# Kernel tuning notes

Hardware: AMD Instinct MI355X
Metric: run time of the kernel (lower is better)

Reference implementation:

```python
import jax, jax.numpy as jnp
import numpy as np

B, S, D_IN, D_OUT = 4, 2048, 2048, 8192


def setup_inputs() -> dict:
    key = jax.random.key(0)
    k1, k2 = jax.random.split(key)
    x = jax.random.normal(k1, (B, S, D_IN), dtype=jnp.float32)
    weight = jax.random.normal(k2, (D_OUT, D_IN), dtype=jnp.float32) * 0.02
    alpha = jnp.float32(1.0)
    bias = jnp.zeros((D_OUT,), dtype=jnp.float32)
    return {"x": x, "weight": weight, "alpha": alpha, "bias": bias}


def reference(x, weight, alpha, bias):
    # Ternary quantization: delta = 0.7 * mean(|w|); w_q in {-1,0,1} * alpha
    delta = 0.7 * jnp.mean(jnp.abs(weight))
    w_t = jnp.where(weight > delta, jnp.float32(1.0),
                    jnp.where(weight < -delta, jnp.float32(-1.0), jnp.float32(0.0)))
    w_q = w_t * alpha  # [out, in]
    # F.linear: x @ w_q^T + bias
    return jnp.einsum('bsd,od->bso', x, w_q) + bias
```

## Files before the change

kernel.cpp:

```cpp
#include <hip/hip_runtime.h>
#include <hip/hip_bf16.h>
#include <stdint.h>

typedef __attribute__((ext_vector_type(4))) int i32x4;
typedef __attribute__((ext_vector_type(16))) int i32x16;
typedef signed char s8;

#define M_TOT 8192
#define N_TOT 8192
#define K_TOT 2048
#define W_COUNT (N_TOT * K_TOT)
#define X_COUNT (M_TOT * K_TOT)

__global__ void tl_reduce(const float* __restrict__ w, const float* __restrict__ x,
                          double* __restrict__ wsum, float* __restrict__ xmax) {
    const int b = blockIdx.x;
    if (b < 1024) {
        const int tid = b * 256 + threadIdx.x;
        const float4* w4 = (const float4*)w;
        double s = 0.0;
        for (int i = tid; i < W_COUNT / 4; i += 1024 * 256) {
            float4 v = w4[i];
            s += (double)fabsf(v.x) + (double)fabsf(v.y) + (double)fabsf(v.z) + (double)fabsf(v.w);
        }
        #pragma unroll
        for (int off = 32; off > 0; off >>= 1) s += __shfl_down(s, off);
        __shared__ double red[4];
        if ((threadIdx.x & 63) == 0) red[threadIdx.x >> 6] = s;
        __syncthreads();
        if (threadIdx.x == 0) wsum[b] = (red[0] + red[1]) + (red[2] + red[3]);
    } else {
        const int tid = (b - 1024) * 256 + threadIdx.x;
        const float4* x4 = (const float4*)x;
        float m = 0.0f;
        for (int i = tid; i < X_COUNT / 4; i += 1024 * 256) {
            float4 v = x4[i];
            m = fmaxf(m, fmaxf(fmaxf(fabsf(v.x), fabsf(v.y)), fmaxf(fabsf(v.z), fabsf(v.w))));
        }
        #pragma unroll
        for (int off = 32; off > 0; off >>= 1) m = fmaxf(m, __shfl_down(m, off));
        __shared__ float redm[4];
        if ((threadIdx.x & 63) == 0) redm[threadIdx.x >> 6] = m;
        __syncthreads();
        if (threadIdx.x == 0) xmax[b - 1024] = fmaxf(fmaxf(redm[0], redm[1]), fmaxf(redm[2], redm[3]));
    }
}

__global__ void tl_finalize(const double* __restrict__ wsum, const float* __restrict__ xmax,
                            const float* __restrict__ alpha,
                            double* __restrict__ delta, float* __restrict__ qp) {
    const int t = threadIdx.x;
    double s = (wsum[t] + wsum[t + 256]) + (wsum[t + 512] + wsum[t + 768]);
    float m = fmaxf(fmaxf(xmax[t], xmax[t + 256]), fmaxf(xmax[t + 512], xmax[t + 768]));
    #pragma unroll
    for (int off = 32; off > 0; off >>= 1) {
        s += __shfl_down(s, off);
        m = fmaxf(m, __shfl_down(m, off));
    }
    __shared__ double rs[4];
    __shared__ float rm[4];
    if ((t & 63) == 0) { rs[t >> 6] = s; rm[t >> 6] = m; }
    __syncthreads();
    if (t == 0) {
        *delta = 0.7 * (((rs[0] + rs[1]) + (rs[2] + rs[3])) / (double)W_COUNT);
        float mm = fmaxf(fmaxf(rm[0], rm[1]), fmaxf(rm[2], rm[3]));
        qp[0] = 127.0f / mm;
        qp[1] = alpha[0] * (mm / 127.0f);
    }
}

__global__ void tl_tern_w(const float* __restrict__ w, const double* __restrict__ delta_p,
                          s8* __restrict__ wb) {
    const double d = *delta_p;
    const int i = (blockIdx.x * 256 + threadIdx.x) * 16;
    union { s8 c[16]; i32x4 v; } o;
    #pragma unroll
    for (int j = 0; j < 16; j += 4) {
        float4 v = *(const float4*)(w + i + j);
        float f[4] = {v.x, v.y, v.z, v.w};
        #pragma unroll
        for (int r = 0; r < 4; ++r) {
            double wd = (double)f[r];
            o.c[j + r] = wd > d ? 1 : (wd < -d ? -1 : 0);
        }
    }
    *(i32x4*)(wb + i) = o.v;
}

__global__ void tl_quant_x(const float* __restrict__ x, const float* __restrict__ qp,
                           s8* __restrict__ xb) {
    const float inv = qp[0];
    const int i = (blockIdx.x * 256 + threadIdx.x) * 16;
    union { s8 c[16]; i32x4 v; } o;
    #pragma unroll
    for (int j = 0; j < 16; j += 4) {
        float4 v = *(const float4*)(x + i + j);
        float f[4] = {v.x, v.y, v.z, v.w};
        #pragma unroll
        for (int r = 0; r < 4; ++r) {
            int q = (int)__builtin_rintf(f[r] * inv);
            q = q > 127 ? 127 : (q < -127 ? -127 : q);
            o.c[j + r] = (s8)q;
        }
    }
    *(i32x4*)(xb + i) = o.v;
}


#define SB    __builtin_amdgcn_sched_barrier(0)
#define BARR  __builtin_amdgcn_s_barrier()
#define LGKM0 asm volatile("s_waitcnt lgkmcnt(0)" ::: "memory")
#define VMW(N) asm volatile("s_waitcnt vmcnt(" #N ")" ::: "memory")

#define GLDS(SRC, DOFF) __builtin_amdgcn_global_load_lds(                      \
    (const __attribute__((address_space(1))) void*)(SRC),                      \
    (__attribute__((address_space(3))) void*)(lds + (DOFF)), 16, 0, 0)

#define RD_A(S, KK) do {                                                       \
    _Pragma("unroll") for (int m_ = 0; m_ < 4; ++m_)                           \
        aF[m_] = *(const i32x4*)(lds + (S) * 16384 + wrOff + m_ * 2048 +       \
                                 (lrd ^ ((KK) * 32)));                         \
} while (0)

#define RD_B(S, KK) do {                                                       \
    _Pragma("unroll") for (int n_ = 0; n_ < 2; ++n_)                           \
        bF[n_] = *(const i32x4*)(lds + 49152 + (S) * 16384 + wcOff + n_ * 2048 + \
                                 (lrd ^ ((KK) * 32)));                         \
} while (0)

#define MM() do {                                                              \
    _Pragma("unroll") for (int m_ = 0; m_ < 4; ++m_)                           \
    _Pragma("unroll") for (int n_ = 0; n_ < 2; ++n_)                           \
        acc[m_][n_] = __builtin_amdgcn_mfma_i32_32x32x32_i8(                   \
            aF[m_], bF[n_], acc[m_][n_], 0, 0, 0);                             \
} while (0)

#define KTILE(S, SSTG, KOFF, DOSTG, GATE) do {                                 \
                            \
    RD_A(S, 0); RD_B(S, 0);                                                    \
    if (DOSTG) { GLDS(aSrc + (KOFF), (SSTG) * 16384 + L);                      \
                 GLDS(aSrc + (KOFF) + 262144, (SSTG) * 16384 + 8192 + L); }    \
    SB; BARR; LGKM0; SB;                                                       \
    __builtin_amdgcn_s_setprio(1); MM(); __builtin_amdgcn_s_setprio(0); SB; BARR; \
                                        \
    RD_A(S, 1); RD_B(S, 1);                                                    \
    if (DOSTG) { GLDS(bSrc + (KOFF), 49152 + (SSTG) * 16384 + L);              \
                 GLDS(bSrc + (KOFF) + 262144, 49152 + (SSTG) * 16384 + 8192 + L); } \
    SB; BARR; LGKM0; SB;                                                       \
    __builtin_amdgcn_s_setprio(1); MM(); __builtin_amdgcn_s_setprio(0); SB;    \
    GATE; BARR;                                                                \
} while (0)

__global__ __launch_bounds__(512, 1) void tl_gemm_i8(
    const s8* __restrict__ A, const s8* __restrict__ Bm,
    const float* __restrict__ qp, const float* __restrict__ bias,
    float* __restrict__ C) {
    __shared__ __attribute__((aligned(128))) char lds[98304];

    const int t = threadIdx.x;
    const int wid = t >> 6;
    const int l = t & 63;
    const int wr = wid >> 2;
    const int wc = wid & 3;

    const int bid = blockIdx.x;
    const int x = bid & 7;
    const int j = bid >> 3;
    const int tm = x * 4 + ((j >> 3) & 3);
    const int tn = (j >> 5) * 8 + (j & 7);
    const int row0 = tm * 256, col0 = tn * 256;

    const int L = t * 16;
    const int off = L ^ (((L >> 7) & 3) << 4);
    const int sr = off >> 6;
    const int kb = off & 63;
    const s8* aSrc = A + (size_t)(row0 + sr) * K_TOT + kb;
    const s8* bSrc = Bm + (size_t)(col0 + sr) * K_TOT + kb;

    const int rl = l & 31, kg = l >> 5;
    const int lrd = rl * 64 + ((kg ^ ((rl >> 1) & 3)) << 4);
    const int wrOff = wr * 8192;
    const int wcOff = wc * 4096;

    i32x16 acc[4][2] = {};
    i32x4 aF[4], bF[2];

    GLDS(aSrc, L);                    GLDS(aSrc + 262144, 8192 + L);
    GLDS(bSrc, 49152 + L);            GLDS(bSrc + 262144, 49152 + 8192 + L);
    GLDS(aSrc + 64, 16384 + L);       GLDS(aSrc + 64 + 262144, 16384 + 8192 + L);
    GLDS(bSrc + 64, 49152 + 16384 + L);
    GLDS(bSrc + 64 + 262144, 49152 + 16384 + 8192 + L);
    VMW(4); BARR;

    int koff = 128;
    #pragma unroll 1
    for (int i = 0; i < 10; ++i) {
        KTILE(0, 2, koff, 1, VMW(4)); koff += 64;
        KTILE(1, 0, koff, 1, VMW(4)); koff += 64;
        KTILE(2, 1, koff, 1, VMW(4)); koff += 64;
    }
    KTILE(0, 0, 0, 0, VMW(0));
    KTILE(1, 0, 0, 0, (void)0);

    const float osc = qp[1];
    #pragma unroll
    for (int m_ = 0; m_ < 4; ++m_) {
        const int crow = row0 + wr * 128 + m_ * 32 + kg * 4;
        #pragma unroll
        for (int n_ = 0; n_ < 2; ++n_) {
            const int ccol = col0 + wc * 64 + n_ * 32 + rl;
            const float bv = bias[ccol];
            #pragma unroll
            for (int r = 0; r < 16; ++r) {
                const int row = crow + (r & 3) + 8 * (r >> 2);
                C[(size_t)row * N_TOT + ccol] = (float)acc[m_][n_][r] * osc + bv;
            }
        }
    }
}

extern "C" void kernel_launch(void* const* d_in, const int* in_sizes, int n_in,
                              void* d_out, int out_size, void* d_ws, size_t ws_size,
                              hipStream_t stream) {
    const float* x     = (const float*)d_in[0];
    const float* wgt   = (const float*)d_in[1];
    const float* alpha = (const float*)d_in[2];
    const float* bias  = (const float*)d_in[3];
    float* out = (float*)d_out;

    char* ws = (char*)d_ws;
    double* wsum = (double*)ws;
    float* xmax  = (float*)(ws + 8192);
    double* delta = (double*)(ws + 12288);
    float* qp     = (float*)(ws + 12304);
    s8* xb = (s8*)(ws + 16384);
    s8* wb = (s8*)(ws + 16384 + (size_t)X_COUNT);

    tl_reduce<<<2048, 256, 0, stream>>>(wgt, x, wsum, xmax);
    tl_finalize<<<1, 256, 0, stream>>>(wsum, xmax, alpha, delta, qp);
    tl_tern_w<<<W_COUNT / (256 * 16), 256, 0, stream>>>(wgt, delta, wb);
    tl_quant_x<<<X_COUNT / (256 * 16), 256, 0, stream>>>(x, qp, xb);
    tl_gemm_i8<<<(M_TOT / 256) * (N_TOT / 256), 512, 0, stream>>>(xb, wb, qp, bias, out);
}
```

Before: 212.3 us.

## Double-buffer LDS fragments in registers and cut barriers per K tile

Restructures the int8 GEMM main loop so the LDS fragment reads for the next half-tile are issued while the MFMAs for the current one run. Fragments are held in two register sets (aP/bP and aN/bN), and a partial lgkmcnt(6) wait replaces full drains. Each K tile now has a single barrier instead of four, with A and B staging issued together after it. In exchange the loop waits for all outstanding global loads each tile, which shortens the prefetch distance. Launch bounds are also raised to 2 blocks per CU, which caps registers next to the 128-register accumulator and risks spills, even though the 96KB LDS per block likely prevents two blocks from fitting.

```diff
diff --git a/kernel.cpp b/kernel.cpp
--- a/kernel.cpp
+++ b/kernel.cpp
@@ -109,49 +109,52 @@
 
 #define SB    __builtin_amdgcn_sched_barrier(0)
 #define BARR  __builtin_amdgcn_s_barrier()
+#define LGKM6 asm volatile("s_waitcnt lgkmcnt(6)" ::: "memory")
 #define LGKM0 asm volatile("s_waitcnt lgkmcnt(0)" ::: "memory")
 #define VMW(N) asm volatile("s_waitcnt vmcnt(" #N ")" ::: "memory")
+#define PRIO1 __builtin_amdgcn_s_setprio(1)
+#define PRIO0 __builtin_amdgcn_s_setprio(0)
 
 #define GLDS(SRC, DOFF) __builtin_amdgcn_global_load_lds(                      \
     (const __attribute__((address_space(1))) void*)(SRC),                      \
     (__attribute__((address_space(3))) void*)(lds + (DOFF)), 16, 0, 0)
 
-#define RD_A(S, KK) do {                                                       \
+#define READ6(AR, BR, S, KK) do {                                              \
     _Pragma("unroll") for (int m_ = 0; m_ < 4; ++m_)                           \
-        aF[m_] = *(const i32x4*)(lds + (S) * 16384 + wrOff + m_ * 2048 +       \
+        AR[m_] = *(const i32x4*)(lds + (S) * 16384 + wrOff + m_ * 2048 +       \
                                  (lrd ^ ((KK) * 32)));                         \
-} while (0)
-
-#define RD_B(S, KK) do {                                                       \
     _Pragma("unroll") for (int n_ = 0; n_ < 2; ++n_)                           \
-        bF[n_] = *(const i32x4*)(lds + 49152 + (S) * 16384 + wcOff + n_ * 2048 + \
+        BR[n_] = *(const i32x4*)(lds + 49152 + (S) * 16384 + wcOff + n_ * 2048 + \
                                  (lrd ^ ((KK) * 32)));                         \
 } while (0)
 
-#define MM() do {                                                              \
+#define MMX(AR, BR) do {                                                       \
     _Pragma("unroll") for (int m_ = 0; m_ < 4; ++m_)                           \
     _Pragma("unroll") for (int n_ = 0; n_ < 2; ++n_)                           \
         acc[m_][n_] = __builtin_amdgcn_mfma_i32_32x32x32_i8(                   \
-            aF[m_], bF[n_], acc[m_][n_], 0, 0, 0);                             \
-} while (0)
-
-#define KTILE(S, SSTG, KOFF, DOSTG, GATE) do {                                 \
-                            \
-    RD_A(S, 0); RD_B(S, 0);                                                    \
-    if (DOSTG) { GLDS(aSrc + (KOFF), (SSTG) * 16384 + L);                      \
-                 GLDS(aSrc + (KOFF) + 262144, (SSTG) * 16384 + 8192 + L); }    \
-    SB; BARR; LGKM0; SB;                                                       \
-    __builtin_amdgcn_s_setprio(1); MM(); __builtin_amdgcn_s_setprio(0); SB; BARR; \
-                                        \
-    RD_A(S, 1); RD_B(S, 1);                                                    \
-    if (DOSTG) { GLDS(bSrc + (KOFF), 49152 + (SSTG) * 16384 + L);              \
-                 GLDS(bSrc + (KOFF) + 262144, 49152 + (SSTG) * 16384 + 8192 + L); } \
-    SB; BARR; LGKM0; SB;                                                       \
-    __builtin_amdgcn_s_setprio(1); MM(); __builtin_amdgcn_s_setprio(0); SB;    \
-    GATE; BARR;                                                                \
-} while (0)
-
-__global__ __launch_bounds__(512, 1) void tl_gemm_i8(
+            AR[m_], BR[n_], acc[m_][n_], 0, 0, 0);                             \
+} while (0)
+
+#define STG_A(SS, KOFF) do {                                                   \
+    GLDS(aSrc + (KOFF), (SS) * 16384 + L);                                     \
+    GLDS(aSrc + (KOFF) + 262144, (SS) * 16384 + 8192 + L);                     \
+} while (0)
+#define STG_B(SS, KOFF) do {                                                   \
+    GLDS(bSrc + (KOFF), 49152 + (SS) * 16384 + L);                             \
+    GLDS(bSrc + (KOFF) + 262144, 49152 + (SS) * 16384 + 8192 + L);             \
+} while (0)
+
+#define TILE(S, SN, SG, KOFF, DOSTG, LAST) do {                                \
+    READ6(aN, bN, S, 1);                                                       \
+    LGKM6; SB; PRIO1; MMX(aP, bP); PRIO0; SB;                                  \
+    VMW(0); BARR; SB;                                                          \
+    if (!(LAST)) READ6(aP, bP, SN, 0);                                         \
+    if (DOSTG) { STG_A(SG, KOFF); STG_B(SG, KOFF); }                           \
+    if (LAST) { LGKM0; } else { LGKM6; }                                       \
+    SB; PRIO1; MMX(aN, bN); PRIO0; SB;                                         \
+} while (0)
+
+__global__ __launch_bounds__(512, 2) void tl_gemm_i8(
     const s8* __restrict__ A, const s8* __restrict__ Bm,
     const float* __restrict__ qp, const float* __restrict__ bias,
     float* __restrict__ C) {
@@ -164,9 +167,9 @@
     const int wc = wid & 3;
 
     const int bid = blockIdx.x;
-    const int x = bid & 7;
+    const int xc = bid & 7;
     const int j = bid >> 3;
-    const int tm = x * 4 + ((j >> 3) & 3);
+    const int tm = xc * 4 + ((j >> 3) & 3);
     const int tn = (j >> 5) * 8 + (j & 7);
     const int row0 = tm * 256, col0 = tn * 256;
 
@@ -183,24 +186,22 @@
     const int wcOff = wc * 4096;
 
     i32x16 acc[4][2] = {};
-    i32x4 aF[4], bF[2];
-
-    GLDS(aSrc, L);                    GLDS(aSrc + 262144, 8192 + L);
-    GLDS(bSrc, 49152 + L);            GLDS(bSrc + 262144, 49152 + 8192 + L);
-    GLDS(aSrc + 64, 16384 + L);       GLDS(aSrc + 64 + 262144, 16384 + 8192 + L);
-    GLDS(bSrc + 64, 49152 + 16384 + L);
-    GLDS(bSrc + 64 + 262144, 49152 + 16384 + 8192 + L);
-    VMW(4); BARR;
+    i32x4 aP[4], bP[2], aN[4], bN[2];
+
+    STG_A(0, 0); STG_B(0, 0);
+    STG_A(1, 64); STG_B(1, 64);
+    VMW(4); BARR; SB;
+    READ6(aP, bP, 0, 0);
 
     int koff = 128;
     #pragma unroll 1
     for (int i = 0; i < 10; ++i) {
-        KTILE(0, 2, koff, 1, VMW(4)); koff += 64;
-        KTILE(1, 0, koff, 1, VMW(4)); koff += 64;
-        KTILE(2, 1, koff, 1, VMW(4)); koff += 64;
-    }
-    KTILE(0, 0, 0, 0, VMW(0));
-    KTILE(1, 0, 0, 0, (void)0);
+        TILE(0, 1, 2, koff, 1, 0); koff += 64;
+        TILE(1, 2, 0, koff, 1, 0); koff += 64;
+        TILE(2, 0, 1, koff, 1, 0); koff += 64;
+    }
+    TILE(0, 1, 0, 0, 0, 0);
+    TILE(1, 1, 0, 0, 0, 1);
 
     const float osc = qp[1];
     #pragma unroll
```

Result: no change. 215.6 us (+1.6%).

## Split each K-tile into four barrier-separated MFMA phases and target two blocks per CU

Applied to the files above, without the earlier changes.

Each 64-wide K step now runs as four phases instead of two. Every phase loads a 2x2 set of A and B fragments from LDS, issues one async global-to-LDS copy and runs four int8 MFMAs. The goal is to spread global loads and LDS reads more finely across the MFMA work and to shrink the fragment register footprint. The launch bound also changes to ask for two 512-thread blocks per CU. In exchange there are twice as many workgroup barriers per K tile. The two-block occupancy hint caps registers near what the 128-register accumulator tile alone needs, which risks spilling, and 96 KB of LDS per block may prevent a second block from fitting anyway.

```diff
diff --git a/kernel.cpp b/kernel.cpp
--- a/kernel.cpp
+++ b/kernel.cpp
@@ -111,47 +111,58 @@
 #define BARR  __builtin_amdgcn_s_barrier()
 #define LGKM0 asm volatile("s_waitcnt lgkmcnt(0)" ::: "memory")
 #define VMW(N) asm volatile("s_waitcnt vmcnt(" #N ")" ::: "memory")
+#define PRIO1 __builtin_amdgcn_s_setprio(1)
+#define PRIO0 __builtin_amdgcn_s_setprio(0)
 
 #define GLDS(SRC, DOFF) __builtin_amdgcn_global_load_lds(                      \
     (const __attribute__((address_space(1))) void*)(SRC),                      \
     (__attribute__((address_space(3))) void*)(lds + (DOFF)), 16, 0, 0)
 
-#define RD_A(S, KK) do {                                                       \
-    _Pragma("unroll") for (int m_ = 0; m_ < 4; ++m_)                           \
-        aF[m_] = *(const i32x4*)(lds + (S) * 16384 + wrOff + m_ * 2048 +       \
-                                 (lrd ^ ((KK) * 32)));                         \
-} while (0)
-
-#define RD_B(S, KK) do {                                                       \
-    _Pragma("unroll") for (int n_ = 0; n_ < 2; ++n_)                           \
-        bF[n_] = *(const i32x4*)(lds + 49152 + (S) * 16384 + wcOff + n_ * 2048 + \
-                                 (lrd ^ ((KK) * 32)));                         \
-} while (0)
-
-#define MM() do {                                                              \
-    _Pragma("unroll") for (int m_ = 0; m_ < 4; ++m_)                           \
-    _Pragma("unroll") for (int n_ = 0; n_ < 2; ++n_)                           \
-        acc[m_][n_] = __builtin_amdgcn_mfma_i32_32x32x32_i8(                   \
-            aF[m_], bF[n_], acc[m_][n_], 0, 0, 0);                             \
-} while (0)
-
-#define KTILE(S, SSTG, KOFF, DOSTG, GATE) do {                                 \
-                            \
-    RD_A(S, 0); RD_B(S, 0);                                                    \
-    if (DOSTG) { GLDS(aSrc + (KOFF), (SSTG) * 16384 + L);                      \
-                 GLDS(aSrc + (KOFF) + 262144, (SSTG) * 16384 + 8192 + L); }    \
-    SB; BARR; LGKM0; SB;                                                       \
-    __builtin_amdgcn_s_setprio(1); MM(); __builtin_amdgcn_s_setprio(0); SB; BARR; \
-                                        \
-    RD_A(S, 1); RD_B(S, 1);                                                    \
-    if (DOSTG) { GLDS(bSrc + (KOFF), 49152 + (SSTG) * 16384 + L);              \
-                 GLDS(bSrc + (KOFF) + 262144, 49152 + (SSTG) * 16384 + 8192 + L); } \
-    SB; BARR; LGKM0; SB;                                                       \
-    __builtin_amdgcn_s_setprio(1); MM(); __builtin_amdgcn_s_setprio(0); SB;    \
+#define RD_A2(AR, S, MB, KK) do {                                              \
+    AR[0] = *(const i32x4*)(lds + (S) * 16384 + wrOff + ((MB) + 0) * 2048 +    \
+                            (lrd ^ ((KK) * 32)));                              \
+    AR[1] = *(const i32x4*)(lds + (S) * 16384 + wrOff + ((MB) + 1) * 2048 +    \
+                            (lrd ^ ((KK) * 32)));                              \
+} while (0)
+#define RD_B2(BR, S, KK) do {                                                  \
+    BR[0] = *(const i32x4*)(lds + 49152 + (S) * 16384 + wcOff + 0 * 2048 +     \
+                            (lrd ^ ((KK) * 32)));                              \
+    BR[1] = *(const i32x4*)(lds + 49152 + (S) * 16384 + wcOff + 1 * 2048 +     \
+                            (lrd ^ ((KK) * 32)));                              \
+} while (0)
+
+#define MM4(AR, BR, MB) do {                                                   \
+    acc[(MB)][0]     = __builtin_amdgcn_mfma_i32_32x32x32_i8(AR[0], BR[0], acc[(MB)][0], 0, 0, 0);     \
+    acc[(MB)][1]     = __builtin_amdgcn_mfma_i32_32x32x32_i8(AR[0], BR[1], acc[(MB)][1], 0, 0, 0);     \
+    acc[(MB) + 1][0] = __builtin_amdgcn_mfma_i32_32x32x32_i8(AR[1], BR[0], acc[(MB) + 1][0], 0, 0, 0); \
+    acc[(MB) + 1][1] = __builtin_amdgcn_mfma_i32_32x32x32_i8(AR[1], BR[1], acc[(MB) + 1][1], 0, 0, 0); \
+} while (0)
+
+#define KT8(S, SG, KOFF, DOSTG, GATE) do {                                     \
+                                                           \
+    RD_A2(aP, S, 0, 0); RD_B2(bC, S, 0);                                       \
+    if (DOSTG) GLDS(aSrc + (KOFF), (SG) * 16384 + L);                          \
+    SB; BARR; LGKM0; SB;                                                       \
+    PRIO1; MM4(aP, bC, 0); PRIO0; BARR;                                        \
+                                \
+    RD_A2(aQ, S, 2, 0); RD_B2(bD, S, 1);                                       \
+    if (DOSTG) GLDS(aSrc + (KOFF) + 262144, (SG) * 16384 + 8192 + L);          \
+    SB; BARR; LGKM0; SB;                                                       \
+    PRIO1; MM4(aQ, bC, 2); PRIO0; BARR;                                        \
+                                                           \
+    RD_A2(aP, S, 0, 1);                                                        \
+    if (DOSTG) GLDS(bSrc + (KOFF), 49152 + (SG) * 16384 + L);                  \
+    SB; BARR; LGKM0; SB;                                                       \
+    PRIO1; MM4(aP, bD, 0); PRIO0; BARR;                                        \
+                                             \
+    RD_A2(aQ, S, 2, 1);                                                        \
+    if (DOSTG) GLDS(bSrc + (KOFF) + 262144, 49152 + (SG) * 16384 + 8192 + L);  \
+    SB; BARR; LGKM0; SB;                                                       \
+    PRIO1; MM4(aQ, bD, 2); PRIO0;                                              \
     GATE; BARR;                                                                \
 } while (0)
 
-__global__ __launch_bounds__(512, 1) void tl_gemm_i8(
+__global__ __launch_bounds__(512, 2) void tl_gemm_i8(
     const s8* __restrict__ A, const s8* __restrict__ Bm,
     const float* __restrict__ qp, const float* __restrict__ bias,
     float* __restrict__ C) {
@@ -164,9 +175,9 @@
     const int wc = wid & 3;
 
     const int bid = blockIdx.x;
-    const int x = bid & 7;
+    const int xc = bid & 7;
     const int j = bid >> 3;
-    const int tm = x * 4 + ((j >> 3) & 3);
+    const int tm = xc * 4 + ((j >> 3) & 3);
     const int tn = (j >> 5) * 8 + (j & 7);
     const int row0 = tm * 256, col0 = tn * 256;
 
@@ -183,24 +194,24 @@
     const int wcOff = wc * 4096;
 
     i32x16 acc[4][2] = {};
-    i32x4 aF[4], bF[2];
-
-    GLDS(aSrc, L);                    GLDS(aSrc + 262144, 8192 + L);
-    GLDS(bSrc, 49152 + L);            GLDS(bSrc + 262144, 49152 + 8192 + L);
-    GLDS(aSrc + 64, 16384 + L);       GLDS(aSrc + 64 + 262144, 16384 + 8192 + L);
+    i32x4 aP[2], aQ[2], bC[2], bD[2];
+
+    GLDS(aSrc, 0 + L);                 GLDS(aSrc + 262144, 8192 + L);
+    GLDS(bSrc, 49152 + L);             GLDS(bSrc + 262144, 49152 + 8192 + L);
+    GLDS(aSrc + 64, 16384 + L);        GLDS(aSrc + 64 + 262144, 16384 + 8192 + L);
     GLDS(bSrc + 64, 49152 + 16384 + L);
     GLDS(bSrc + 64 + 262144, 49152 + 16384 + 8192 + L);
-    VMW(4); BARR;
+    VMW(4); SB; BARR;
 
     int koff = 128;
     #pragma unroll 1
     for (int i = 0; i < 10; ++i) {
-        KTILE(0, 2, koff, 1, VMW(4)); koff += 64;
-        KTILE(1, 0, koff, 1, VMW(4)); koff += 64;
-        KTILE(2, 1, koff, 1, VMW(4)); koff += 64;
-    }
-    KTILE(0, 0, 0, 0, VMW(0));
-    KTILE(1, 0, 0, 0, (void)0);
+        KT8(0, 2, koff, 1, VMW(4)); koff += 64;
+        KT8(1, 0, koff, 1, VMW(4)); koff += 64;
+        KT8(2, 1, koff, 1, VMW(4)); koff += 64;
+    }
+    KT8(0, 0, 0, 0, VMW(0));
+    KT8(1, 0, 0, 0, (void)0);
 
     const float osc = qp[1];
     #pragma unroll
```

Measured after the change: 212.1 us. No clear change (-0.1%).
